# Performance work log

Measured on AMD Instinct MI355X. Metric: run time of the kernel, lower is better.

## Reference

```python
import jax, jax.numpy as jnp
import numpy as np

K, D, B, T = 512, 256, 32, 4096

def setup_inputs() -> dict:
    key = jax.random.key(0)
    k1, k2 = jax.random.split(key)
    z_e_x = jax.random.normal(k1, (B, D, T), dtype=jnp.float32)
    # nn.Embedding weight init uniform(-1/K, 1/K)
    emb_weight = jax.random.uniform(k2, (K, D), dtype=jnp.float32, minval=-1.0 / K, maxval=1.0 / K)
    return {"z_e_x": z_e_x, "emb_weight": emb_weight}

def reference(z_e_x, emb_weight):
    # forward(): permute [B,D,T] -> [B,T,D], nearest-codebook indices
    z = jnp.transpose(z_e_x, (0, 2, 1))  # [B, T, D]
    # squared L2 distances: ||z||^2 - 2 z.W^T + ||W||^2  -> [B, T, K]
    z_sq = jnp.sum(z * z, axis=-1, keepdims=True)           # [B, T, 1]
    w_sq = jnp.sum(emb_weight * emb_weight, axis=-1)        # [K]
    cross = jnp.einsum('btd,kd->btk', z, emb_weight)        # [B, T, K]
    dists = z_sq - 2.0 * cross + w_sq[None, None, :]
    latents = jnp.argmin(dists, axis=-1)                    # [B, T] int
    return latents
```

## Files before the change

kernel.cpp:

```cpp
#include <hip/hip_runtime.h>
#include <math.h>

#define NK 512
#define DD 256
#define NB 32
#define NT 4096

typedef __attribute__((ext_vector_type(8))) _Float16 f16x8;
typedef __attribute__((ext_vector_type(4))) float f32x4;

#define MARGIN 1.5e-4f
#define DCH 16
#define NCH 16
#define ASTR 536
#define PCAP   524288
#define PBCAP  2048
#define ZCROWS 65536
#define ZCMAX  48

__device__ __forceinline__ unsigned short f16bits(float x) {
    _Float16 h = (_Float16)x;
    unsigned short s;
    __builtin_memcpy(&s, &h, 2);
    return s;
}

__global__ __launch_bounds__(512) void prep_kernel(const float* __restrict__ W,
                                                   unsigned short* __restrict__ Wpp,
                                                   float* __restrict__ wsq,
                                                   int* __restrict__ gcnt,
                                                   int* __restrict__ pcnt,
                                                   int* __restrict__ oflow) {
    const int bx = blockIdx.x;
    const int k  = threadIdx.x;
    if (bx < NCH) {
        const int d0 = bx * DCH;
        float w[16];
        const float4* src4 = (const float4*)(W + (size_t)k * DD + d0);
        #pragma unroll
        for (int q = 0; q < 4; ++q) {
            float4 v = src4[q];
            w[4 * q + 0] = v.x; w[4 * q + 1] = v.y; w[4 * q + 2] = v.z; w[4 * q + 3] = v.w;
        }
        __align__(16) unsigned int dw[16];
        #pragma unroll
        for (int j = 0; j < 16; ++j) {
            unsigned short s = f16bits(w[j] * 4096.0f);
            dw[j] = (unsigned int)s | ((unsigned int)s << 16);
        }
        unsigned short* dst = Wpp + ((size_t)bx * 512 + k) * 32;
        #pragma unroll
        for (int j = 0; j < 4; ++j) ((int4*)dst)[j] = ((const int4*)dw)[j];
    } else {
        const float4* row = (const float4*)(W + (size_t)k * DD);
        double s = 0.0;
        #pragma unroll 8
        for (int i = 0; i < DD / 4; ++i) {
            float4 v = row[i];
            s += (double)v.x * v.x + (double)v.y * v.y + (double)v.z * v.z + (double)v.w * v.w;
        }
        wsq[k] = (float)s;
        if (k == 0) *gcnt = 0;
        if (k == 1) *pcnt = 0;
        if (k == 2) *oflow = 0;
    }
}

__global__ __launch_bounds__(256, 2) void vq_phase1(const float* __restrict__ Z,
                                                    const unsigned short* __restrict__ Wpp,
                                                    const float* __restrict__ wsq,
                                                    int* __restrict__ out,
                                                    int* __restrict__ gties,
                                                    int* __restrict__ gcnt,
                                                    float* __restrict__ Zc,
                                                    float* __restrict__ zq,
                                                    unsigned long long* __restrict__ slots,
                                                    int* __restrict__ gpairs,
                                                    int* __restrict__ pcnt,
                                                    int* __restrict__ oflow) {
    __shared__ __align__(16) short As[64 * ASTR];
    __shared__ int lcnt, gbase, pcl, pbase_sh;

    const int tid  = threadIdx.x;
    const int wave = tid >> 6;
    const int lane = tid & 63;
    const int lm   = lane & 15;
    const int lq   = lane >> 4;
    const int nw   = wave;

    const int bx = blockIdx.x;
    const int b  = bx >> 6;
    const int t0 = (bx & 63) * 64;

    const int t_l = tid & 63;
    const int dgs = tid >> 6;

    const float* zcol = Z + (size_t)b * DD * NT + t0 + t_l;

    if (tid == 0) { lcnt = 0; pcl = 0; }

    double zacc = 0.0;
    #pragma unroll
    for (int half = 0; half < 2; ++half) {
        float zv[32];
        #pragma unroll
        for (int j = 0; j < 32; ++j)
            zv[j] = zcol[(size_t)(dgs * 64 + half * 32 + j) * NT];
        #pragma unroll
        for (int j = 0; j < 32; ++j)
            zacc = fma((double)zv[j], (double)zv[j], zacc);
        #pragma unroll
        for (int j0 = 0; j0 < 32; j0 += 4) {
            __align__(16) unsigned int u[4];
            #pragma unroll
            for (int q = 0; q < 4; ++q) {
                float z = zv[j0 + q];
                _Float16 zh = (_Float16)z;
                float rz = z - (float)zh;
                unsigned short hs, ls;
                __builtin_memcpy(&hs, &zh, 2);
                ls = f16bits(rz);
                u[q] = (unsigned int)hs | ((unsigned int)ls << 16);
            }
            *(int4*)&As[t_l * ASTR + (dgs * 64 + half * 32 + j0) * 2] = *(const int4*)u;
        }
    }
    __syncthreads();

    const unsigned short* wb = Wpp + ((size_t)(nw * 128 + lm) * 32) + lq * 8;

    f32x4 acc[4][8];
    #pragma unroll
    for (int mt = 0; mt < 4; ++mt)
        #pragma unroll
        for (int nt = 0; nt < 8; ++nt)
            acc[mt][nt] = (f32x4){0.f, 0.f, 0.f, 0.f};

    int4 bv0[8], bv1[8];
    #pragma unroll
    for (int nt = 0; nt < 8; ++nt)
        bv0[nt] = *(const int4*)(wb + nt * 512);

    #pragma unroll
    for (int c = 0; c < NCH; ++c) {
        int4* cur = (c & 1) ? bv1 : bv0;
        int4* nxt = (c & 1) ? bv0 : bv1;
        if (c < NCH - 1) {
            const unsigned short* wp = wb + (size_t)(c + 1) * 16384;
            #pragma unroll
            for (int nt = 0; nt < 8; ++nt)
                nxt[nt] = *(const int4*)(wp + nt * 512);
        }
        f16x8 a[4];
        #pragma unroll
        for (int mt = 0; mt < 4; ++mt)
            a[mt] = *(const f16x8*)&As[(mt * 16 + lm) * ASTR + c * 32 + lq * 8];
        #pragma unroll
        for (int mt = 0; mt < 4; ++mt)
            #pragma unroll
            for (int nt = 0; nt < 8; ++nt)
                acc[mt][nt] = __builtin_amdgcn_mfma_f32_16x16x32_f16(
                    a[mt], *(const f16x8*)&cur[nt], acc[mt][nt], 0, 0, 0);
    }

    __syncthreads();
    char* base = (char*)As;
    double* zred  = (double*)base;
    float*  zf    = (float*)(base + 2048);
    float*  qf    = (float*)(base + 2304);
    int*    tia   = (int*)(base + 2560);
    int*    ltok  = (int*)(base + 2816);
    float*  cb1   = (float*)(base + 3072);
    float*  cb2   = (float*)(base + 4096);
    int*    cbi   = (int*)(base + 5120);
    int*    plist = (int*)(base + 6144);
    float*  colbuf = (float*)(base + 14336);

    zred[dgs * 64 + t_l] = zacc;
    __syncthreads();
    if (tid < 64) {
        double s = zred[tid];
        #pragma unroll
        for (int p = 1; p < 4; ++p) s += zred[p * 64 + tid];
        zf[tid] = (float)s;
    }
    __syncthreads();

    float wq[8];
    #pragma unroll
    for (int nt = 0; nt < 8; ++nt)
        wq[nt] = wsq[nw * 128 + nt * 16 + lm];
    const int kbase = nw * 128 + lm;

    #pragma unroll
    for (int mt = 0; mt < 4; ++mt) {
        #pragma unroll
        for (int r = 0; r < 4; ++r) {
            float zz = zf[mt * 16 + lq * 4 + r];
            float q1 = INFINITY, q2 = INFINITY;
            int i1 = 0x7fffffff;
            #pragma unroll
            for (int nt = 0; nt < 8; ++nt) {
                float c2   = __fmul_rn(acc[mt][nt][r], 4.8828125e-4f);
                float dist = __fadd_rn(__fsub_rn(zz, c2), wq[nt]);
                int kk = kbase + nt * 16;
                if (dist < q1 || (dist == q1 && kk < i1)) { q2 = q1; q1 = dist; i1 = kk; }
                else if (dist < q2) q2 = dist;
            }
            #pragma unroll
            for (int mk = 1; mk <= 8; mk <<= 1) {
                float o1 = __shfl_xor(q1, mk);
                float o2 = __shfl_xor(q2, mk);
                int   oi = __shfl_xor(i1, mk);
                if (o1 < q1 || (o1 == q1 && oi < i1)) { q2 = fminf(q1, o2); q1 = o1; i1 = oi; }
                else { q2 = fminf(o1, q2); }
            }
            if (lm == 0) {
                int m = mt * 16 + lq * 4 + r;
                cb1[m * 4 + nw] = q1;
                cb2[m * 4 + nw] = q2;
                cbi[m * 4 + nw] = i1;
            }
        }
    }
    __syncthreads();
    if (tid < 64) {
        float q1 = cb1[tid * 4], q2 = cb2[tid * 4];
        int   i1 = cbi[tid * 4];
        #pragma unroll
        for (int p = 1; p < 4; ++p) {
            float c1 = cb1[tid * 4 + p], c2v = cb2[tid * 4 + p];
            int   ci = cbi[tid * 4 + p];
            if (c1 < q1 || (c1 == q1 && ci < i1)) { q2 = fminf(q1, c2v); q1 = c1; i1 = ci; }
            else { q2 = fminf(q2, c1); }
        }
        out[(size_t)b * NT + t0 + tid] = i1;
        qf[tid] = q1;
        int ta = -1;
        if (q2 - q1 <= MARGIN) {
            ta = atomicAdd(&lcnt, 1);
            ltok[ta] = tid;
        }
        tia[tid] = ta;
    }
    __syncthreads();
    const int nloc = lcnt;
    if (nloc == 0) return;

    if (tid == 0) gbase = atomicAdd(gcnt, nloc);
    __syncthreads();

    if (tid < nloc) gties[gbase + tid] = b * NT + t0 + ltok[tid];

    const bool okzc = (gbase + nloc <= ZCROWS) && (nloc <= ZCMAX);
    if (!okzc) {
        if (tid == 0) *oflow = 1;
        return;
    }
    if (tid < nloc) slots[gbase + tid] = 0xFFFFFFFFFFFFFFFFULL;

    #pragma unroll
    for (int mt = 0; mt < 4; ++mt) {
        #pragma unroll
        for (int r = 0; r < 4; ++r) {
            const int tok = mt * 16 + lq * 4 + r;
            const int ta  = tia[tok];
            if (ta < 0) continue;
            const int ti  = gbase + ta;
            const float thr = qf[tok] + MARGIN;
            const float zz  = zf[tok];
            #pragma unroll
            for (int nt = 0; nt < 8; ++nt) {
                float c2   = __fmul_rn(acc[mt][nt][r], 4.8828125e-4f);
                float dist = __fadd_rn(__fsub_rn(zz, c2), wq[nt]);
                if (dist <= thr) {
                    int p = atomicAdd(&pcl, 1);
                    if (p < PBCAP) plist[p] = (ti << 9) | (kbase + nt * 16);
                }
            }
        }
    }
    __syncthreads();
    if (tid == 0) {
        int take = pcl;
        int bs = atomicAdd(pcnt, take);
        pbase_sh = bs;
        if (take > PBCAP || bs + take > PCAP) *oflow = 1;
    }
    __syncthreads();
    {
        int take = pcl; if (take > PBCAP) take = PBCAP;
        for (int j = tid; j < take; j += 256) {
            int gp = pbase_sh + j;
            if (gp < PCAP) gpairs[gp] = plist[j];
        }
    }

    {
        const int i  = tid & 63;
        const int dw = tid >> 6;
        for (int du = 0; du < 64; ++du) {
            const int d = du * 4 + dw;
            if (i < nloc)
                colbuf[i * 257 + d] =
                    Z[(size_t)b * DD * NT + (size_t)d * NT + (t0 + ltok[i])];
        }
    }
    __syncthreads();
    for (int i = 0; i < nloc; ++i)
        Zc[(size_t)(gbase + i) * 256 + tid] = colbuf[i * 257 + tid];
    if (tid < nloc) {
        const float* cp = colbuf + tid * 257;
        double tot = 0.0;
        for (int seg = 0; seg < 32; ++seg) {
            double s = 0.0;
            #pragma unroll
            for (int jj = 0; jj < 8; ++jj) {
                double zz = (double)cp[seg * 8 + jj];
                s = fma(zz, zz, s);
            }
            tot += s;
        }
        zq[gbase + tid] = (float)tot;
    }
}

__global__ __launch_bounds__(256) void vq_fix_pairs(const float* __restrict__ W,
                                                    const float* __restrict__ wsq,
                                                    const float* __restrict__ Zc,
                                                    const float* __restrict__ zq,
                                                    const int* __restrict__ gpairs,
                                                    const int* __restrict__ pcnt,
                                                    unsigned long long* __restrict__ slots) {
    int np = *pcnt;
    if (np > PCAP) np = PCAP;
    for (int j = blockIdx.x * 256 + threadIdx.x; j < np; j += (int)gridDim.x * 256) {
        const int p  = gpairs[j];
        const int ti = p >> 9;
        const int k  = p & 511;
        if (ti >= ZCROWS) continue;
        const float4* zr = (const float4*)(Zc + (size_t)ti * 256);
        const float4* wr = (const float4*)(W + (size_t)k * DD);
        float a8 = 0.f;
        #pragma unroll 4
        for (int q = 0; q < 64; ++q) {
            float4 w4 = wr[q];
            float4 z4 = zr[q];
            a8 = fmaf(z4.x, w4.x, a8);
            a8 = fmaf(z4.y, w4.y, a8);
            a8 = fmaf(z4.z, w4.z, a8);
            a8 = fmaf(z4.w, w4.w, a8);
        }
        float da = __fadd_rn(__fsub_rn(zq[ti], __fmul_rn(2.0f, a8)), wsq[k]);
        unsigned long long key =
            ((unsigned long long)__float_as_uint(da) << 32) | (unsigned int)k;
        atomicMin(&slots[ti], key);
    }
}

__global__ __launch_bounds__(256) void vq_final(const int* __restrict__ gties,
                                                const int* __restrict__ gcnt,
                                                const int* __restrict__ oflow,
                                                const unsigned long long* __restrict__ slots,
                                                int* __restrict__ out) {
    if (*oflow) return;
    const int n = *gcnt;
    for (int j = blockIdx.x * 256 + threadIdx.x; j < n; j += (int)gridDim.x * 256) {
        out[gties[j]] = (int)(slots[j] & 511ULL);
    }
}

__global__ __launch_bounds__(256) void vq_fix(const float* __restrict__ Z,
                                              const float* __restrict__ W,
                                              const float* __restrict__ wsq,
                                              const int* __restrict__ gties,
                                              const int* __restrict__ gcnt,
                                              int* __restrict__ out,
                                              const int* __restrict__ oflow) {
    if (oflow != nullptr && *oflow == 0) return;

    __shared__ __align__(16) float Zs[8][256];
    __shared__ double pz[8][32];
    __shared__ float  zsqs[8];
    __shared__ int    bts[8];
    __shared__ float  rv[8][4];
    __shared__ int    ri[8][4];

    const int tid  = threadIdx.x;
    const int lane = tid & 63;
    const int wvx  = tid >> 6;
    const int n    = *gcnt;

    for (int base = blockIdx.x * 8; base < n; base += (int)gridDim.x * 8) {
        const int m = (n - base < 8) ? (n - base) : 8;
        __syncthreads();
        if (tid < 8) bts[tid] = gties[base + ((tid < m) ? tid : 0)];
        __syncthreads();

        #pragma unroll
        for (int i = 0; i < 8; ++i) {
            if (i < m) {
                int tb = bts[i];
                int bb = tb >> 12, t = tb & 4095;
                Zs[i][tid] = Z[(size_t)bb * DD * NT + (size_t)tid * NT + t];
            }
        }
        __syncthreads();

        {
            int i = tid >> 5, seg = tid & 31;
            double s = 0.0;
            #pragma unroll
            for (int j = 0; j < 8; ++j) {
                double zz = (double)Zs[i][seg * 8 + j];
                s = fma(zz, zz, s);
            }
            pz[i][seg] = s;
        }
        __syncthreads();
        if (tid < 8) {
            double s = 0.0;
            #pragma unroll
            for (int j = 0; j < 32; ++j) s += pz[tid][j];
            zsqs[tid] = (float)s;
        }
        __syncthreads();

        float da[2][8];
        #pragma unroll
        for (int rr = 0; rr < 2; ++rr) {
            int k = tid + rr * 256;
            const float4* wr = (const float4*)(W + (size_t)k * DD);
            float a8[8];
            #pragma unroll
            for (int i = 0; i < 8; ++i) a8[i] = 0.f;
            #pragma unroll 2
            for (int q = 0; q < 64; ++q) {
                float4 w4 = wr[q];
                #pragma unroll
                for (int i = 0; i < 8; ++i) {
                    float4 z4 = *(const float4*)&Zs[i][4 * q];
                    a8[i] = fmaf(z4.x, w4.x, a8[i]);
                    a8[i] = fmaf(z4.y, w4.y, a8[i]);
                    a8[i] = fmaf(z4.z, w4.z, a8[i]);
                    a8[i] = fmaf(z4.w, w4.w, a8[i]);
                }
            }
            float wqv = wsq[k];
            #pragma unroll
            for (int i = 0; i < 8; ++i)
                da[rr][i] = __fadd_rn(__fsub_rn(zsqs[i], __fmul_rn(2.0f, a8[i])), wqv);
        }

        #pragma unroll
        for (int i = 0; i < 8; ++i) {
            float v = da[0][i]; int ix = tid;
            if (da[1][i] < v) { v = da[1][i]; ix = tid + 256; }
            #pragma unroll
            for (int mk = 1; mk <= 32; mk <<= 1) {
                float ov = __shfl_xor(v, mk);
                int   oi = __shfl_xor(ix, mk);
                if (ov < v || (ov == v && oi < ix)) { v = ov; ix = oi; }
            }
            if (lane == 0) { rv[i][wvx] = v; ri[i][wvx] = ix; }
        }
        __syncthreads();
        if (tid < 8 && tid < m) {
            float v = INFINITY; int ix = 0x7fffffff;
            #pragma unroll
            for (int w = 0; w < 4; ++w) {
                if (rv[tid][w] < v || (rv[tid][w] == v && ri[tid][w] < ix)) {
                    v = rv[tid][w]; ix = ri[tid][w];
                }
            }
            out[bts[tid]] = ix;
        }
    }
}

__global__ __launch_bounds__(256, 2) void vq_phase1_reg(const float* __restrict__ Z,
                                                        const unsigned short* __restrict__ Wpp,
                                                        const float* __restrict__ wsq,
                                                        int* __restrict__ out,
                                                        int* __restrict__ gties,
                                                        int* __restrict__ gcnt) {
    __shared__ __align__(16) short As[64 * ASTR];
    __shared__ int lcnt, gbase;

    const int tid  = threadIdx.x;
    const int wave = tid >> 6;
    const int lane = tid & 63;
    const int lm   = lane & 15;
    const int lq   = lane >> 4;
    const int nw   = wave;

    const int bx = blockIdx.x;
    const int b  = bx >> 6;
    const int t0 = (bx & 63) * 64;

    const int t_l = tid & 63;
    const int dgs = tid >> 6;

    const float* zcol = Z + (size_t)b * DD * NT + t0 + t_l;

    if (tid == 0) lcnt = 0;

    double zacc = 0.0;
    #pragma unroll
    for (int half = 0; half < 2; ++half) {
        float zv[32];
        #pragma unroll
        for (int j = 0; j < 32; ++j)
            zv[j] = zcol[(size_t)(dgs * 64 + half * 32 + j) * NT];
        #pragma unroll
        for (int j = 0; j < 32; ++j)
            zacc = fma((double)zv[j], (double)zv[j], zacc);
        #pragma unroll
        for (int j0 = 0; j0 < 32; j0 += 4) {
            __align__(16) unsigned int u[4];
            #pragma unroll
            for (int q = 0; q < 4; ++q) {
                float z = zv[j0 + q];
                _Float16 zh = (_Float16)z;
                float rz = z - (float)zh;
                unsigned short hs, ls;
                __builtin_memcpy(&hs, &zh, 2);
                ls = f16bits(rz);
                u[q] = (unsigned int)hs | ((unsigned int)ls << 16);
            }
            *(int4*)&As[t_l * ASTR + (dgs * 64 + half * 32 + j0) * 2] = *(const int4*)u;
        }
    }
    __syncthreads();

    const unsigned short* wb = Wpp + ((size_t)(nw * 128 + lm) * 32) + lq * 8;

    f32x4 acc[4][8];
    #pragma unroll
    for (int mt = 0; mt < 4; ++mt)
        #pragma unroll
        for (int nt = 0; nt < 8; ++nt)
            acc[mt][nt] = (f32x4){0.f, 0.f, 0.f, 0.f};

    int4 bv0[8], bv1[8];
    #pragma unroll
    for (int nt = 0; nt < 8; ++nt)
        bv0[nt] = *(const int4*)(wb + nt * 512);

    #pragma unroll
    for (int c = 0; c < NCH; ++c) {
        int4* cur = (c & 1) ? bv1 : bv0;
        int4* nxt = (c & 1) ? bv0 : bv1;
        if (c < NCH - 1) {
            const unsigned short* wp = wb + (size_t)(c + 1) * 16384;
            #pragma unroll
            for (int nt = 0; nt < 8; ++nt)
                nxt[nt] = *(const int4*)(wp + nt * 512);
        }
        f16x8 a[4];
        #pragma unroll
        for (int mt = 0; mt < 4; ++mt)
            a[mt] = *(const f16x8*)&As[(mt * 16 + lm) * ASTR + c * 32 + lq * 8];
        #pragma unroll
        for (int mt = 0; mt < 4; ++mt)
            #pragma unroll
            for (int nt = 0; nt < 8; ++nt)
                acc[mt][nt] = __builtin_amdgcn_mfma_f32_16x16x32_f16(
                    a[mt], *(const f16x8*)&cur[nt], acc[mt][nt], 0, 0, 0);
    }

    __syncthreads();
    double* zred = (double*)As;
    float*  zf   = (float*)(As + 1024);
    float*  cb1  = (float*)(As + 1536);
    float*  cb2  = (float*)(As + 2048);
    int*    cbi  = (int*)(As + 2560);
    int*    llist = (int*)(As + 3072);

    zred[dgs * 64 + t_l] = zacc;
    __syncthreads();
    if (tid < 64) {
        double s = zred[tid];
        #pragma unroll
        for (int p = 1; p < 4; ++p) s += zred[p * 64 + tid];
        zf[tid] = (float)s;
    }
    __syncthreads();

    float wq[8];
    #pragma unroll
    for (int nt = 0; nt < 8; ++nt)
        wq[nt] = wsq[nw * 128 + nt * 16 + lm];
    const int kbase = nw * 128 + lm;

    #pragma unroll
    for (int mt = 0; mt < 4; ++mt) {
        #pragma unroll
        for (int r = 0; r < 4; ++r) {
            float zz = zf[mt * 16 + lq * 4 + r];
            float q1 = INFINITY, q2 = INFINITY;
            int i1 = 0x7fffffff;
            #pragma unroll
            for (int nt = 0; nt < 8; ++nt) {
                float c2   = __fmul_rn(acc[mt][nt][r], 4.8828125e-4f);
                float dist = __fadd_rn(__fsub_rn(zz, c2), wq[nt]);
                int kk = kbase + nt * 16;
                if (dist < q1 || (dist == q1 && kk < i1)) { q2 = q1; q1 = dist; i1 = kk; }
                else if (dist < q2) q2 = dist;
            }
            #pragma unroll
            for (int mk = 1; mk <= 8; mk <<= 1) {
                float o1 = __shfl_xor(q1, mk);
                float o2 = __shfl_xor(q2, mk);
                int   oi = __shfl_xor(i1, mk);
                if (o1 < q1 || (o1 == q1 && oi < i1)) { q2 = fminf(q1, o2); q1 = o1; i1 = oi; }
                else { q2 = fminf(o1, q2); }
            }
            if (lm == 0) {
                int m = mt * 16 + lq * 4 + r;
                cb1[m * 4 + nw] = q1;
                cb2[m * 4 + nw] = q2;
                cbi[m * 4 + nw] = i1;
            }
        }
    }
    __syncthreads();
    if (tid < 64) {
        float q1 = cb1[tid * 4], q2 = cb2[tid * 4];
        int   i1 = cbi[tid * 4];
        #pragma unroll
        for (int p = 1; p < 4; ++p) {
            float c1 = cb1[tid * 4 + p], c2v = cb2[tid * 4 + p];
            int   ci = cbi[tid * 4 + p];
            if (c1 < q1 || (c1 == q1 && ci < i1)) { q2 = fminf(q1, c2v); q1 = c1; i1 = ci; }
            else { q2 = fminf(q2, c1); }
        }
        out[(size_t)b * NT + t0 + tid] = i1;
        if (q2 - q1 <= MARGIN) {
            int p = atomicAdd(&lcnt, 1);
            llist[p] = b * NT + t0 + tid;
        }
    }
    __syncthreads();
    if (tid == 0) gbase = (lcnt > 0) ? atomicAdd(gcnt, lcnt) : 0;
    __syncthreads();
    if (tid < lcnt) gties[gbase + tid] = llist[tid];
}

#define BT 128
#define BK 128
#define DCHUNK 32
#define NKC (NK / BK)
#define NDC (DD / DCHUNK)
#define WSTR (BK + 4)

__global__ __launch_bounds__(256) void vq_fallback(const float* __restrict__ Z,
                                                   const float* __restrict__ W,
                                                   int* __restrict__ out) {
    __shared__ __align__(16) float Zs[DCHUNK * BT];
    __shared__ __align__(16) float Ws[DCHUNK * WSTR];
    __shared__ float wsqs[NK];

    const int tid = threadIdx.x;
    const int tx  = tid & 15;
    const int ty  = tid >> 4;
    const int b   = blockIdx.y;
    const int t0  = blockIdx.x * BT;

    for (int k = tid; k < NK; k += 256) {
        const float4* row = (const float4*)(W + (size_t)k * DD);
        double s = 0.0;
        for (int i = 0; i < DD / 4; ++i) {
            float4 v = row[i];
            s += (double)v.x * v.x + (double)v.y * v.y + (double)v.z * v.z + (double)v.w * v.w;
        }
        wsqs[k] = (float)s;
    }

    const float* Zb = Z + (size_t)b * DD * NT + t0;

    float best[8]; int bidx[8];
    #pragma unroll
    for (int a = 0; a < 8; ++a) { best[a] = INFINITY; bidx[a] = 0x7fffffff; }
    double zsqd[8];
    #pragma unroll
    for (int a = 0; a < 8; ++a) zsqd[a] = 0.0;
    float zsqf[8];

    for (int kc = 0; kc < NKC; ++kc) {
        float acc[8][8];
        #pragma unroll
        for (int a = 0; a < 8; ++a)
            #pragma unroll
            for (int c = 0; c < 8; ++c) acc[a][c] = 0.f;

        for (int dc = 0; dc < NDC; ++dc) {
            const int d0 = dc * DCHUNK;
            __syncthreads();
            #pragma unroll
            for (int i = 0; i < 4; ++i) {
                int f  = tid + i * 256;
                int r  = f >> 5;
                int c4 = f & 31;
                float4 v = *(const float4*)(Zb + (size_t)(d0 + r) * NT + c4 * 4);
                *(float4*)(&Zs[r * BT + c4 * 4]) = v;
            }
            #pragma unroll
            for (int i = 0; i < 4; ++i) {
                int u  = tid + i * 256;
                int k  = u >> 3;
                int rg = u & 7;
                float4 v = *(const float4*)(W + (size_t)(kc * BK + k) * DD + d0 + rg * 4);
                Ws[(rg * 4 + 0) * WSTR + k] = v.x;
                Ws[(rg * 4 + 1) * WSTR + k] = v.y;
                Ws[(rg * 4 + 2) * WSTR + k] = v.z;
                Ws[(rg * 4 + 3) * WSTR + k] = v.w;
            }
            __syncthreads();
            #pragma unroll 4
            for (int d = 0; d < DCHUNK; ++d) {
                float4 z0 = *(const float4*)(&Zs[d * BT + ty * 8]);
                float4 z1 = *(const float4*)(&Zs[d * BT + ty * 8 + 4]);
                float4 w0 = *(const float4*)(&Ws[d * WSTR + tx * 8]);
                float4 w1 = *(const float4*)(&Ws[d * WSTR + tx * 8 + 4]);
                float za[8] = {z0.x, z0.y, z0.z, z0.w, z1.x, z1.y, z1.z, z1.w};
                float wa[8] = {w0.x, w0.y, w0.z, w0.w, w1.x, w1.y, w1.z, w1.w};
                if (kc == 0) {
                    #pragma unroll
                    for (int a = 0; a < 8; ++a)
                        zsqd[a] = fma((double)za[a], (double)za[a], zsqd[a]);
                }
                #pragma unroll
                for (int a = 0; a < 8; ++a)
                    #pragma unroll
                    for (int c = 0; c < 8; ++c)
                        acc[a][c] = fmaf(za[a], wa[c], acc[a][c]);
            }
        }
        if (kc == 0) {
            #pragma unroll
            for (int a = 0; a < 8; ++a) zsqf[a] = (float)zsqd[a];
        }
        #pragma unroll
        for (int c = 0; c < 8; ++c) {
            int   kg = kc * BK + tx * 8 + c;
            float wqv = wsqs[kg];
            #pragma unroll
            for (int a = 0; a < 8; ++a) {
                float c2   = __fmul_rn(2.0f, acc[a][c]);
                float s    = __fsub_rn(zsqf[a], c2);
                float dist = __fadd_rn(s, wqv);
                if (dist < best[a] || (dist == best[a] && kg < bidx[a])) {
                    best[a] = dist; bidx[a] = kg;
                }
            }
        }
    }
    __syncthreads();
    float* redv = Zs;
    int*   redi = (int*)Ws;
    #pragma unroll
    for (int a = 0; a < 8; ++a) {
        int tl2 = ty * 8 + a;
        redv[tl2 * 16 + tx] = best[a];
        redi[tl2 * 16 + tx] = bidx[a];
    }
    __syncthreads();
    if (tid < BT) {
        float bv = INFINITY; int bi = 0x7fffffff;
        #pragma unroll
        for (int j = 0; j < 16; ++j) {
            float v = redv[tid * 16 + j];
            int   i = redi[tid * 16 + j];
            if (v < bv || (v == bv && i < bi)) { bv = v; bi = i; }
        }
        out[(size_t)b * NT + t0 + tid] = bi;
    }
}

extern "C" void kernel_launch(void* const* d_in, const int* in_sizes, int n_in,
                              void* d_out, int out_size, void* d_ws, size_t ws_size,
                              hipStream_t stream) {
    const float* Z = (const float*)d_in[0];
    const float* W = (const float*)d_in[1];
    int* out = (int*)d_out;

    const size_t OFF_WSQ  = 0;
    const size_t OFF_CNT  = 2048;
    const size_t OFF_PCNT = 2052;
    const size_t OFF_OFL  = 2056;
    const size_t OFF_ZQ   = 4096;
    const size_t OFF_WPP  = OFF_ZQ + 524288;
    const size_t OFF_TIE  = OFF_WPP + 524288;
    const size_t OFF_SLOT = OFF_TIE + 524288;
    const size_t OFF_PAIR = OFF_SLOT + 1048576;
    const size_t OFF_ZC   = OFF_PAIR + (size_t)PCAP * 4;
    const size_t NEED_BIG = OFF_ZC + (size_t)ZCROWS * 1024;

    const size_t T2_WSQ = 0;
    const size_t T2_CNT = 2048;
    const size_t T2_WPP = 4096;
    const size_t T2_TIE = T2_WPP + 524288;
    const size_t NEED_T2 = T2_TIE + 524288;

    if (ws_size >= NEED_BIG) {
        float* wsq  = (float*)((char*)d_ws + OFF_WSQ);
        int*   gcnt = (int*)((char*)d_ws + OFF_CNT);
        int*   pcnt = (int*)((char*)d_ws + OFF_PCNT);
        int*   ofl  = (int*)((char*)d_ws + OFF_OFL);
        float* zq   = (float*)((char*)d_ws + OFF_ZQ);
        unsigned short* wpp = (unsigned short*)((char*)d_ws + OFF_WPP);
        int*   gties = (int*)((char*)d_ws + OFF_TIE);
        unsigned long long* slots = (unsigned long long*)((char*)d_ws + OFF_SLOT);
        int*   gpairs = (int*)((char*)d_ws + OFF_PAIR);
        float* zc   = (float*)((char*)d_ws + OFF_ZC);

        prep_kernel<<<dim3(NCH + 1), dim3(512), 0, stream>>>(W, wpp, wsq, gcnt, pcnt, ofl);
        vq_phase1<<<dim3(2048), dim3(256), 0, stream>>>(Z, wpp, wsq, out, gties, gcnt,
                                                        zc, zq, slots, gpairs, pcnt, ofl);
        vq_fix_pairs<<<dim3(512), dim3(256), 0, stream>>>(W, wsq, zc, zq, gpairs, pcnt, slots);
        vq_fix<<<dim3(256), dim3(256), 0, stream>>>(Z, W, wsq, gties, gcnt, out, ofl);
        vq_final<<<dim3(256), dim3(256), 0, stream>>>(gties, gcnt, ofl, slots, out);
    } else if (ws_size >= NEED_T2) {
        float* wsq  = (float*)((char*)d_ws + T2_WSQ);
        int*   gcnt = (int*)((char*)d_ws + T2_CNT);
        unsigned short* wpp = (unsigned short*)((char*)d_ws + T2_WPP);
        int*   gties = (int*)((char*)d_ws + T2_TIE);

        prep_kernel<<<dim3(NCH + 1), dim3(512), 0, stream>>>(W, wpp, wsq, gcnt, gcnt, gcnt);
        vq_phase1_reg<<<dim3(2048), dim3(256), 0, stream>>>(Z, wpp, wsq, out, gties, gcnt);
        vq_fix<<<dim3(256), dim3(256), 0, stream>>>(Z, W, wsq, gties, gcnt, out, nullptr);
    } else {
        vq_fallback<<<dim3(NT / BT, NB), dim3(256), 0, stream>>>(Z, W, out);
    }
}
```

Measured before the change: 358.9 us.

## Move tie-token column gather and norm out of phase1 into separate kernel

The strided gather of Z columns for near-tie tokens and their double-precision norm computation move out of the tail of the main MFMA kernel into a new vq_gather kernel, one wave per tie token. This removes a serial, poorly coalesced tail from the blocks that have ties and drops the per-block ZCMAX cap. The cost is an extra kernel launch, and the scattered column reads remain. vq_fix_pairs now also checks the overflow flag.

Measured after the change: 339.2 us, median of 2. 1.06x faster.

```diff
diff --git a/kernel.cpp b/kernel.cpp
--- a/kernel.cpp
+++ b/kernel.cpp
@@ -16,7 +16,6 @@
 #define PCAP   524288
 #define PBCAP  2048
 #define ZCROWS 65536
-#define ZCMAX  48
 
 __device__ __forceinline__ unsigned short f16bits(float x) {
     _Float16 h = (_Float16)x;
@@ -72,8 +71,6 @@
                                                     int* __restrict__ out,
                                                     int* __restrict__ gties,
                                                     int* __restrict__ gcnt,
-                                                    float* __restrict__ Zc,
-                                                    float* __restrict__ zq,
                                                     unsigned long long* __restrict__ slots,
                                                     int* __restrict__ gpairs,
                                                     int* __restrict__ pcnt,
@@ -174,7 +171,6 @@
     float*  cb2   = (float*)(base + 4096);
     int*    cbi   = (int*)(base + 5120);
     int*    plist = (int*)(base + 6144);
-    float*  colbuf = (float*)(base + 14336);
 
     zred[dgs * 64 + t_l] = zacc;
     __syncthreads();
@@ -250,14 +246,16 @@
     if (tid == 0) gbase = atomicAdd(gcnt, nloc);
     __syncthreads();
 
-    if (tid < nloc) gties[gbase + tid] = b * NT + t0 + ltok[tid];
-
-    const bool okzc = (gbase + nloc <= ZCROWS) && (nloc <= ZCMAX);
+    if (tid < nloc) {
+        gties[gbase + tid] = b * NT + t0 + ltok[tid];
+        slots[gbase + tid] = 0xFFFFFFFFFFFFFFFFULL;
+    }
+
+    const bool okzc = (gbase + nloc <= ZCROWS);
     if (!okzc) {
         if (tid == 0) *oflow = 1;
         return;
     }
-    if (tid < nloc) slots[gbase + tid] = 0xFFFFFFFFFFFFFFFFULL;
 
     #pragma unroll
     for (int mt = 0; mt < 4; ++mt) {
@@ -295,33 +293,63 @@
             if (gp < PCAP) gpairs[gp] = plist[j];
         }
     }
-
-    {
-        const int i  = tid & 63;
-        const int dw = tid >> 6;
-        for (int du = 0; du < 64; ++du) {
-            const int d = du * 4 + dw;
-            if (i < nloc)
-                colbuf[i * 257 + d] =
-                    Z[(size_t)b * DD * NT + (size_t)d * NT + (t0 + ltok[i])];
-        }
-    }
-    __syncthreads();
-    for (int i = 0; i < nloc; ++i)
-        Zc[(size_t)(gbase + i) * 256 + tid] = colbuf[i * 257 + tid];
-    if (tid < nloc) {
-        const float* cp = colbuf + tid * 257;
-        double tot = 0.0;
-        for (int seg = 0; seg < 32; ++seg) {
+}
+
+__global__ __launch_bounds__(256) void vq_gather(const float* __restrict__ Z,
+                                                 const int* __restrict__ gties,
+                                                 const int* __restrict__ gcnt,
+                                                 const int* __restrict__ oflow,
+                                                 float* __restrict__ Zc,
+                                                 float* __restrict__ zq) {
+    if (*oflow) return;
+    const int n = *gcnt;
+    if (n == 0) return;
+
+    __shared__ float  col[4][256];
+    __shared__ double pz[4][32];
+
+    const int tid  = threadIdx.x;
+    const int wv   = tid >> 6;
+    const int lane = tid & 63;
+    const int nwv  = (int)gridDim.x * 4;
+    const int iters = (n + nwv - 1) / nwv;
+
+    for (int it = 0; it < iters; ++it) {
+        const int ti  = (blockIdx.x * 4 + wv) + it * nwv;
+        const bool act = (ti < n);
+        if (act) {
+            const int bt = gties[ti];
+            const int bb = bt >> 12, t = bt & 4095;
+            const float* zp = Z + (size_t)bb * DD * NT + t;
+            float v[4];
+            #pragma unroll
+            for (int j = 0; j < 4; ++j) {
+                v[j] = zp[(size_t)(lane + 64 * j) * NT];
+                col[wv][lane + 64 * j] = v[j];
+            }
+            #pragma unroll
+            for (int j = 0; j < 4; ++j)
+                Zc[(size_t)ti * 256 + lane + 64 * j] = v[j];
+        }
+        __syncthreads();
+        if (act && lane < 32) {
+            const float* cp = &col[wv][lane * 8];
             double s = 0.0;
             #pragma unroll
             for (int jj = 0; jj < 8; ++jj) {
-                double zz = (double)cp[seg * 8 + jj];
+                double zz = (double)cp[jj];
                 s = fma(zz, zz, s);
             }
-            tot += s;
-        }
-        zq[gbase + tid] = (float)tot;
+            pz[wv][lane] = s;
+        }
+        __syncthreads();
+        if (act && lane == 0) {
+            double tot = 0.0;
+            #pragma unroll
+            for (int sg = 0; sg < 32; ++sg) tot += pz[wv][sg];
+            zq[ti] = (float)tot;
+        }
+        __syncthreads();
     }
 }
 
@@ -331,7 +359,9 @@
                                                     const float* __restrict__ zq,
                                                     const int* __restrict__ gpairs,
                                                     const int* __restrict__ pcnt,
+                                                    const int* __restrict__ oflow,
                                                     unsigned long long* __restrict__ slots) {
+    if (*oflow) return;
     int np = *pcnt;
     if (np > PCAP) np = PCAP;
     for (int j = blockIdx.x * 256 + threadIdx.x; j < np; j += (int)gridDim.x * 256) {
@@ -817,8 +847,9 @@
 
         prep_kernel<<<dim3(NCH + 1), dim3(512), 0, stream>>>(W, wpp, wsq, gcnt, pcnt, ofl);
         vq_phase1<<<dim3(2048), dim3(256), 0, stream>>>(Z, wpp, wsq, out, gties, gcnt,
-                                                        zc, zq, slots, gpairs, pcnt, ofl);
-        vq_fix_pairs<<<dim3(512), dim3(256), 0, stream>>>(W, wsq, zc, zq, gpairs, pcnt, slots);
+                                                        slots, gpairs, pcnt, ofl);
+        vq_gather<<<dim3(512), dim3(256), 0, stream>>>(Z, gties, gcnt, ofl, zc, zq);
+        vq_fix_pairs<<<dim3(512), dim3(256), 0, stream>>>(W, wsq, zc, zq, gpairs, pcnt, ofl, slots);
         vq_fix<<<dim3(256), dim3(256), 0, stream>>>(Z, W, wsq, gties, gcnt, out, ofl);
         vq_final<<<dim3(256), dim3(256), 0, stream>>>(gties, gcnt, ofl, slots, out);
     } else if (ws_size >= NEED_T2) {
```
